# Performance work log

Measured on AMD Instinct MI355X. Metric: run time of the kernel, lower is better.

Reference implementation:

```python
import jax, jax.numpy as jnp
import numpy as np

N_NODES = 512
STATE_DIM = 16
MESSAGE_DIM = 32
HID_MSG = 64
HID_RO = 64
N_STEPS = 5


def setup_inputs() -> dict:
    key = jax.random.key(0)
    ks = jax.random.split(key, 16)
    s, m, hm, hr = STATE_DIM, MESSAGE_DIM, HID_MSG, HID_RO
    gru_in = s + m
    k_gru = 1.0 / np.sqrt(s)
    inp = {
        'J': jax.random.normal(ks[0], (N_NODES, N_NODES), jnp.float32),
        'b': jax.random.normal(ks[1], (N_NODES,), jnp.float32),
        # message MLP (torch init: weight ~ N(0, 0.1), bias = 0)
        'W1': 0.1 * jax.random.normal(ks[2], (hm, 2 * s + 3), jnp.float32),
        'b1': jnp.zeros((hm,), jnp.float32),
        'W2': 0.1 * jax.random.normal(ks[3], (hm, hm), jnp.float32),
        'b2': jnp.zeros((hm,), jnp.float32),
        'W3': 0.1 * jax.random.normal(ks[4], (m, hm), jnp.float32),
        'b3': jnp.zeros((m,), jnp.float32),
        # GRUCell params (torch default: U(-1/sqrt(hidden), 1/sqrt(hidden)))
        'W_ih': jax.random.uniform(ks[5], (3 * s, gru_in), jnp.float32, -k_gru, k_gru),
        'b_ih': jnp.zeros((3 * s,), jnp.float32),
        'W_hh': jax.random.uniform(ks[6], (3 * s, s), jnp.float32, -k_gru, k_gru),
        'b_hh': jnp.zeros((3 * s,), jnp.float32),
        # readout MLP
        'Wr1': 0.1 * jax.random.normal(ks[7], (hr, s), jnp.float32),
        'br1': jnp.zeros((hr,), jnp.float32),
        'Wr2': 0.1 * jax.random.normal(ks[8], (hr, hr), jnp.float32),
        'br2': jnp.zeros((hr,), jnp.float32),
        'Wr3': 0.1 * jax.random.normal(ks[9], (2, hr), jnp.float32),
        'br3': jnp.zeros((2,), jnp.float32),
    }
    return inp


def _gru_cell(x, h, W_ih, b_ih, W_hh, b_hh):
    s = h.shape[-1]
    gi = x @ W_ih.T + b_ih  # (n, 3s)
    gh = h @ W_hh.T + b_hh  # (n, 3s)
    ir, iz, in_ = gi[:, :s], gi[:, s:2 * s], gi[:, 2 * s:]
    hr, hz, hn = gh[:, :s], gh[:, s:2 * s], gh[:, 2 * s:]
    r = jax.nn.sigmoid(ir + hr)
    z = jax.nn.sigmoid(iz + hz)
    n = jnp.tanh(in_ + r * hn)
    return (1.0 - z) * n + z * h


def reference(J, b, W1, b1, W2, b2, W3, b3, W_ih, b_ih, W_hh, b_hh,
              Wr1, br1, Wr2, br2, Wr3, br3):
    n = J.shape[0]
    s = W_hh.shape[1]
    # Split first message-MLP layer by input blocks [h_i | h_j | J_ij | b_i | b_j]
    # so we never materialize the (n, n, 2s+3) feature tensor.
    W1_hi = W1[:, :s]            # (hm, s)
    W1_hj = W1[:, s:2 * s]       # (hm, s)
    w_J = W1[:, 2 * s]           # (hm,)
    w_bi = W1[:, 2 * s + 1]      # (hm,)
    w_bj = W1[:, 2 * s + 2]      # (hm,)
    # static per-pair part of layer-1 preactivation: (n, n, hm)
    static1 = (J[:, :, None] * w_J
               + b[:, None, None] * w_bi
               + b[None, :, None] * w_bj
               + b1)

    h0 = jnp.zeros((n, s), jnp.float32)

    def step(h, _):
        pre = (h @ W1_hi.T)[:, None, :] + (h @ W1_hj.T)[None, :, :] + static1
        x = jax.nn.relu(pre)                      # (n, n, hm)
        x = jax.nn.relu(x @ W2.T + b2)            # (n, n, hm)
        msg = x @ W3.T + b3                       # (n, n, m)
        m_j = msg.sum(axis=0)                     # sum over i -> (n, m)
        gru_in = jnp.concatenate([h, m_j], axis=1)
        h_new = _gru_cell(gru_in, h, W_ih, b_ih, W_hh, b_hh)
        return h_new, None

    h, _ = jax.lax.scan(step, h0, None, length=N_STEPS)

    y = jax.nn.relu(h @ Wr1.T + br1)
    y = jax.nn.relu(y @ Wr2.T + br2)
    y = jax.nn.sigmoid(y @ Wr3.T + br3)           # (n, 2)
    y = y / jnp.sum(y, axis=1, keepdims=True)
    return y
```

## Files before the change

### kernel.cpp

```cpp
#include <hip/hip_runtime.h>
#include <hip/hip_bf16.h>

#define NSTEPS 5
#define ABUFSZ 32768

typedef __attribute__((ext_vector_type(8))) short short8;
typedef __attribute__((ext_vector_type(4))) float floatx4;

static __device__ __forceinline__ unsigned pk2bf(float a, float b) {
    __hip_bfloat162 h = __float22bfloat162_rn(make_float2(a, b));
    return *reinterpret_cast<unsigned*>(&h);
}

static __device__ __forceinline__ void store_wt4(float* addr, floatx4 v) {
    __asm__ volatile("global_store_dwordx4 %0, %1, off sc0 sc1"
                     :: "v"(addr), "v"(v) : "memory");
}
static __device__ __forceinline__ void store_wt1(float* addr, float v) {
    __asm__ volatile("global_store_dword %0, %1, off sc0 sc1"
                     :: "v"(addr), "v"(v) : "memory");
}

struct Params {
    const float *J, *b, *W1, *b1, *W2, *b2, *W3, *b3;
    const float *W_ih, *b_ih, *W_hh, *b_hh;
    const float *Wr1, *br1, *Wr2, *br2, *Wr3, *br3;
    float *out;
    float *aBase;
    float *Jt;
    unsigned *bar;
};

static __device__ __forceinline__ void gbar(unsigned* bar, unsigned ph) {
    __builtin_amdgcn_s_waitcnt(0);
    __syncthreads();
    if (threadIdx.x == 0) {
        const int g = blockIdx.x & 7;
        unsigned old = __hip_atomic_fetch_add(&bar[g * 16], 1u, __ATOMIC_RELAXED,
                                              __HIP_MEMORY_SCOPE_AGENT);
        if (old == 64u * ph - 1u) {
            unsigned mo = __hip_atomic_fetch_add(&bar[128], 1u, __ATOMIC_RELAXED,
                                                 __HIP_MEMORY_SCOPE_AGENT);
            if (mo == 8u * ph - 1u)
                __hip_atomic_store(&bar[144], ph, __ATOMIC_RELAXED,
                                   __HIP_MEMORY_SCOPE_AGENT);
        }
        while (__hip_atomic_load(&bar[144], __ATOMIC_RELAXED,
                                 __HIP_MEMORY_SCOPE_AGENT) < ph)
            __builtin_amdgcn_s_sleep(2);
    }
    __syncthreads();
    __asm__ volatile("" ::: "memory");
}

__global__ __launch_bounds__(256, 2) void ggnn_fused(Params p)
{
    const int tid = threadIdx.x;
    const int l = tid & 63, w = tid >> 6;
    const int m = l & 15, q = l >> 4;
    const int j = blockIdx.x;

    __shared__ __align__(16) float smTile[64][65];
    __shared__ __align__(16) float smJ[512];
    __shared__ __align__(16) float smW1hi[64][16];
    __shared__ __align__(16) float smW1hj[64][16];
    __shared__ __align__(16) float smwJ[64], smwbi[64], smwbj[64], smb1[64];
    __shared__ __align__(16) float smC[64];
    __shared__ __align__(16) float smA[64];
    __shared__ __align__(16) float smH[16];
    __shared__ __align__(16) float smWave[4][64];
    __shared__ __align__(16) float smMacc[64];
    __shared__ __align__(16) float smGin[48];
    __shared__ __align__(16) float smGi[48], smGh[48];
    __shared__ __align__(16) float smY[64], smY2[64];
    __shared__ float smR[2];

    if (blockIdx.x < 64) {
        int ti = blockIdx.x >> 3, tj = blockIdx.x & 7;
        for (int pp = 0; pp < 16; ++pp) {
            int e = pp * 256 + tid; int r = e >> 6, c = e & 63;
            smTile[r][c] = p.J[(ti * 64 + r) * 512 + tj * 64 + c];
        }
        __syncthreads();
        for (int pp = 0; pp < 16; ++pp) {
            int e = pp * 256 + tid; int r = e >> 6, c = e & 63;
            store_wt1(p.Jt + (tj * 64 + r) * 512 + ti * 64 + c, smTile[c][r]);
        }
    }

    if (tid < 64) {
        int o = tid;
        #pragma unroll
        for (int s = 0; s < 16; ++s) {
            smW1hi[o][s] = p.W1[o * 35 + s];
            smW1hj[o][s] = p.W1[o * 35 + 16 + s];
        }
        smwJ[o]  = p.W1[o * 35 + 32];
        smwbi[o] = p.W1[o * 35 + 33];
        smwbj[o] = p.W1[o * 35 + 34];
        smb1[o]  = p.b1[o];
    }

    short8 bfw[4][2];
    float b2n[4];
    {
        const floatx4* W2v = (const floatx4*)p.W2;
        #pragma unroll
        for (int nt = 0; nt < 4; ++nt) {
            int n = nt * 16 + m;
            #pragma unroll
            for (int ks = 0; ks < 2; ++ks) {
                int kb = ks * 32 + q * 8;
                floatx4 f0 = W2v[n * 16 + (kb >> 2)];
                floatx4 f1 = W2v[n * 16 + (kb >> 2) + 1];
                union { short8 s; unsigned u[4]; } t;
                t.u[0] = pk2bf(f0[0], f0[1]); t.u[1] = pk2bf(f0[2], f0[3]);
                t.u[2] = pk2bf(f1[0], f1[1]); t.u[3] = pk2bf(f1[2], f1[3]);
                bfw[nt][ks] = t.s;
            }
            b2n[nt] = p.b2[nt * 16 + m];
        }
    }
    __syncthreads();

    const float bj = p.b[j];

    floatx4 wva, wvb, wvc, wvd;
    {
        const floatx4* wv4 = (const floatx4*)smwJ;
        wva = wv4[q * 2];     wvb = wv4[q * 2 + 1];
        wvc = wv4[8 + q * 2]; wvd = wv4[8 + q * 2 + 1];
    }

    if (tid < 64) smC[tid] = bj * smwbj[tid] + smb1[tid];
    if (tid < 16) {
        floatx4 v;
        #pragma unroll
        for (int e = 0; e < 4; ++e) v[e] = bj * smwbi[tid * 4 + e];
        store_wt4(p.aBase + j * 64 + tid * 4, v);
        smH[tid] = 0.f;
    }

    gbar(p.bar, 1);

    if (tid < 128) ((floatx4*)smJ)[tid] = ((const floatx4*)p.Jt)[j * 128 + tid];
    __syncthreads();

    for (int t = 0; t < NSTEPS; ++t) {
        const float* aIn = p.aBase + t * ABUFSZ;
        const floatx4* c4 = (const floatx4*)smC;
        floatx4 cva = c4[q*2], cvb = c4[q*2+1], cvc = c4[8+q*2], cvd = c4[8+q*2+1];

        floatx4 acc[4];
        #pragma unroll
        for (int nt = 0; nt < 4; ++nt) acc[nt] = (floatx4){0.f,0.f,0.f,0.f};

        const floatx4* a4 = (const floatx4*)aIn;

        for (int c8 = 0; c8 < 8; ++c8) {
            int i = w * 128 + c8 * 16 + m;
            float Jij = smJ[i];
            floatx4 av0 = a4[i*16 + q*2],     av1 = a4[i*16 + q*2 + 1];
            floatx4 av2 = a4[i*16 + 8 + q*2], av3 = a4[i*16 + 8 + q*2 + 1];
            floatx4 x0, x1, x2, x3;
            #pragma unroll
            for (int e = 0; e < 4; ++e) {
                x0[e] = fmaxf(fmaf(Jij, wva[e], av0[e]) + cva[e], 0.f);
                x1[e] = fmaxf(fmaf(Jij, wvb[e], av1[e]) + cvb[e], 0.f);
                x2[e] = fmaxf(fmaf(Jij, wvc[e], av2[e]) + cvc[e], 0.f);
                x3[e] = fmaxf(fmaf(Jij, wvd[e], av3[e]) + cvd[e], 0.f);
            }
            union { short8 s; unsigned u[4]; } fa0, fa1;
            fa0.u[0] = pk2bf(x0[0], x0[1]); fa0.u[1] = pk2bf(x0[2], x0[3]);
            fa0.u[2] = pk2bf(x1[0], x1[1]); fa0.u[3] = pk2bf(x1[2], x1[3]);
            fa1.u[0] = pk2bf(x2[0], x2[1]); fa1.u[1] = pk2bf(x2[2], x2[3]);
            fa1.u[2] = pk2bf(x3[0], x3[1]); fa1.u[3] = pk2bf(x3[2], x3[3]);
            #pragma unroll
            for (int nt = 0; nt < 4; ++nt) {
                floatx4 d = {0.f,0.f,0.f,0.f};
                d = __builtin_amdgcn_mfma_f32_16x16x32_bf16(fa0.s, bfw[nt][0], d, 0, 0, 0);
                d = __builtin_amdgcn_mfma_f32_16x16x32_bf16(fa1.s, bfw[nt][1], d, 0, 0, 0);
                #pragma unroll
                for (int r = 0; r < 4; ++r)
                    acc[nt][r] += fmaxf(d[r] + b2n[nt], 0.f);
            }
        }

        #pragma unroll
        for (int nt = 0; nt < 4; ++nt) {
            float v = acc[nt][0] + acc[nt][1] + acc[nt][2] + acc[nt][3];
            v += __shfl_xor(v, 16);
            v += __shfl_xor(v, 32);
            if (l < 16) smWave[w][nt*16 + l] = v;
        }
        if (tid < 16) smGin[tid] = smH[tid];
        __syncthreads();
        if (tid < 64) smMacc[tid] = smWave[0][tid] + smWave[1][tid]
                                  + smWave[2][tid] + smWave[3][tid];
        __syncthreads();

        {
            int o = tid >> 3, pp = tid & 7;
            const floatx4* W3v = (const floatx4*)p.W3;
            floatx4 wv0 = W3v[o*16 + pp*2], wv1 = W3v[o*16 + pp*2 + 1];
            float part = 0.f;
            #pragma unroll
            for (int e = 0; e < 4; ++e) {
                part = fmaf(wv0[e], smMacc[pp*8 + e], part);
                part = fmaf(wv1[e], smMacc[pp*8 + 4 + e], part);
            }
            part += __shfl_xor(part, 1);
            part += __shfl_xor(part, 2);
            part += __shfl_xor(part, 4);
            if (pp == 0) smGin[16 + o] = part + 512.f * p.b3[o];
        }
        __syncthreads();

        if (tid < 192) {
            int o = tid >> 2, pp = tid & 3;
            const floatx4* Wv = (const floatx4*)p.W_ih;
            floatx4 w0 = Wv[o*12 + pp*3], w1 = Wv[o*12 + pp*3 + 1], w2 = Wv[o*12 + pp*3 + 2];
            int k0 = pp * 12;
            float part = 0.f;
            #pragma unroll
            for (int e = 0; e < 4; ++e) {
                part = fmaf(w0[e], smGin[k0 + e], part);
                part = fmaf(w1[e], smGin[k0 + 4 + e], part);
                part = fmaf(w2[e], smGin[k0 + 8 + e], part);
            }
            part += __shfl_xor(part, 1);
            part += __shfl_xor(part, 2);
            if (pp == 0) smGi[o] = part + p.b_ih[o];
        } else if (tid < 240) {
            int o = tid - 192;
            const floatx4* Wv = (const floatx4*)p.W_hh;
            floatx4 w0 = Wv[o*4], w1 = Wv[o*4+1], w2 = Wv[o*4+2], w3 = Wv[o*4+3];
            float s = p.b_hh[o];
            #pragma unroll
            for (int e = 0; e < 4; ++e) {
                s = fmaf(w0[e], smGin[e],      s);
                s = fmaf(w1[e], smGin[4 + e],  s);
                s = fmaf(w2[e], smGin[8 + e],  s);
                s = fmaf(w3[e], smGin[12 + e], s);
            }
            smGh[o] = s;
        }
        __syncthreads();

        if (tid < 16) {
            float r = 1.f / (1.f + __expf(-(smGi[tid] + smGh[tid])));
            float z = 1.f / (1.f + __expf(-(smGi[16+tid] + smGh[16+tid])));
            float n = tanhf(smGi[32+tid] + r * smGh[32+tid]);
            smH[tid] = (1.f - z) * n + z * smGin[tid];
        }
        __syncthreads();

        if (t < NSTEPS - 1) {
            if (tid < 128) {
                int o = tid & 63, sel = tid >> 6;
                const floatx4* Wv = (const floatx4*)(sel ? &smW1hj[0][0] : &smW1hi[0][0]);
                const floatx4* h4 = (const floatx4*)smH;
                floatx4 w0 = Wv[o*4], w1 = Wv[o*4+1], w2 = Wv[o*4+2], w3 = Wv[o*4+3];
                float s = 0.f;
                #pragma unroll
                for (int e = 0; e < 4; ++e) {
                    s = fmaf(w0[e], h4[0][e], s);
                    s = fmaf(w1[e], h4[1][e], s);
                    s = fmaf(w2[e], h4[2][e], s);
                    s = fmaf(w3[e], h4[3][e], s);
                }
                if (sel == 0) smA[o] = s + bj * smwbi[o];
                else          smC[o] = s + bj * smwbj[o] + smb1[o];
            }
            __syncthreads();
            if (tid < 16) {
                float* aNext = p.aBase + (t + 1) * ABUFSZ;
                store_wt4(aNext + j * 64 + tid * 4, ((floatx4*)smA)[tid]);
            }
            gbar(p.bar, (unsigned)(t + 2));
        }
    }

    if (tid < 64) {
        const floatx4* Wv = (const floatx4*)p.Wr1;
        const floatx4* h4 = (const floatx4*)smH;
        floatx4 w0 = Wv[tid*4], w1 = Wv[tid*4+1], w2 = Wv[tid*4+2], w3 = Wv[tid*4+3];
        float s = p.br1[tid];
        #pragma unroll
        for (int e = 0; e < 4; ++e) {
            s = fmaf(w0[e], h4[0][e], s);
            s = fmaf(w1[e], h4[1][e], s);
            s = fmaf(w2[e], h4[2][e], s);
            s = fmaf(w3[e], h4[3][e], s);
        }
        smY[tid] = fmaxf(s, 0.f);
    }
    __syncthreads();
    {
        int o = tid >> 2, pp = tid & 3;
        const floatx4* Wv = (const floatx4*)p.Wr2;
        const floatx4* y4 = (const floatx4*)smY;
        floatx4 w0 = Wv[o*16 + pp*4],     w1 = Wv[o*16 + pp*4 + 1];
        floatx4 w2 = Wv[o*16 + pp*4 + 2], w3 = Wv[o*16 + pp*4 + 3];
        float part = 0.f;
        #pragma unroll
        for (int e = 0; e < 4; ++e) {
            part = fmaf(w0[e], y4[pp*4][e] * 0.f + smY[pp*16 + e],      part);
            part = fmaf(w1[e], smY[pp*16 + 4 + e],  part);
            part = fmaf(w2[e], smY[pp*16 + 8 + e],  part);
            part = fmaf(w3[e], smY[pp*16 + 12 + e], part);
        }
        part += __shfl_xor(part, 1);
        part += __shfl_xor(part, 2);
        if (pp == 0) smY2[o] = fmaxf(part + p.br2[o], 0.f);
    }
    __syncthreads();
    if (tid < 128) {
        int ot = tid >> 6, pp = tid & 63;
        float part = p.Wr3[ot*64 + pp] * smY2[pp];
        part += __shfl_xor(part, 1);
        part += __shfl_xor(part, 2);
        part += __shfl_xor(part, 4);
        part += __shfl_xor(part, 8);
        part += __shfl_xor(part, 16);
        part += __shfl_xor(part, 32);
        if (pp == 0) smR[ot] = part + p.br3[ot];
    }
    __syncthreads();
    if (tid == 0) {
        float e0 = 1.f / (1.f + __expf(-smR[0]));
        float e1 = 1.f / (1.f + __expf(-smR[1]));
        float tsum = e0 + e1;
        p.out[j*2]     = e0 / tsum;
        p.out[j*2 + 1] = e1 / tsum;
    }
}

extern "C" void kernel_launch(void* const* d_in, const int* in_sizes, int n_in,
                              void* d_out, int out_size, void* d_ws, size_t ws_size,
                              hipStream_t stream)
{
    Params par;
    par.J    = (const float*)d_in[0];
    par.b    = (const float*)d_in[1];
    par.W1   = (const float*)d_in[2];
    par.b1   = (const float*)d_in[3];
    par.W2   = (const float*)d_in[4];
    par.b2   = (const float*)d_in[5];
    par.W3   = (const float*)d_in[6];
    par.b3   = (const float*)d_in[7];
    par.W_ih = (const float*)d_in[8];
    par.b_ih = (const float*)d_in[9];
    par.W_hh = (const float*)d_in[10];
    par.b_hh = (const float*)d_in[11];
    par.Wr1  = (const float*)d_in[12];
    par.br1  = (const float*)d_in[13];
    par.Wr2  = (const float*)d_in[14];
    par.br2  = (const float*)d_in[15];
    par.Wr3  = (const float*)d_in[16];
    par.br3  = (const float*)d_in[17];
    par.out  = (float*)d_out;

    float* ws = (float*)d_ws;
    par.aBase = ws;
    par.Jt    = ws + NSTEPS * ABUFSZ;
    par.bar   = (unsigned*)(ws + NSTEPS * ABUFSZ + 262144);

    hipMemsetAsync(par.bar, 0, 1024, stream);
    hipLaunchKernelGGL(ggnn_fused, dim3(512), dim3(256), 0, stream, par);
}
```

Before: 163.8 us.

## Drop J transpose pre-pass and initial grid barrier; use 512-thread blocks

Removes the cooperative J transpose through global memory along with the first grid-wide barrier. Each block now reads its column of J directly with strided loads and keeps b in shared memory. Step 0 computes the h=0 layer-1 preactivation locally from b_i instead of reading a global buffer. Blocks grow to 512 threads (8 waves), so each wave processes half as many rows, and the wave reduction and W3 matvec are adjusted to match. This cuts one grid barrier and a global round trip, at the cost of uncoalesced column loads and higher register pressure under the new launch bounds.

```diff
diff --git a/kernel.cpp b/kernel.cpp
--- a/kernel.cpp
+++ b/kernel.cpp
@@ -14,10 +14,6 @@
 
 static __device__ __forceinline__ void store_wt4(float* addr, floatx4 v) {
     __asm__ volatile("global_store_dwordx4 %0, %1, off sc0 sc1"
-                     :: "v"(addr), "v"(v) : "memory");
-}
-static __device__ __forceinline__ void store_wt1(float* addr, float v) {
-    __asm__ volatile("global_store_dword %0, %1, off sc0 sc1"
                      :: "v"(addr), "v"(v) : "memory");
 }
 
@@ -27,7 +23,6 @@
     const float *Wr1, *br1, *Wr2, *br2, *Wr3, *br3;
     float *out;
     float *aBase;
-    float *Jt;
     unsigned *bar;
 };
 
@@ -53,41 +48,30 @@
     __asm__ volatile("" ::: "memory");
 }
 
-__global__ __launch_bounds__(256, 2) void ggnn_fused(Params p)
+__global__ __launch_bounds__(512, 4) void ggnn_fused(Params p)
 {
     const int tid = threadIdx.x;
     const int l = tid & 63, w = tid >> 6;
     const int m = l & 15, q = l >> 4;
     const int j = blockIdx.x;
 
-    __shared__ __align__(16) float smTile[64][65];
     __shared__ __align__(16) float smJ[512];
+    __shared__ __align__(16) float smB[512];
     __shared__ __align__(16) float smW1hi[64][16];
     __shared__ __align__(16) float smW1hj[64][16];
     __shared__ __align__(16) float smwJ[64], smwbi[64], smwbj[64], smb1[64];
     __shared__ __align__(16) float smC[64];
     __shared__ __align__(16) float smA[64];
     __shared__ __align__(16) float smH[16];
-    __shared__ __align__(16) float smWave[4][64];
+    __shared__ __align__(16) float smWave[8][64];
     __shared__ __align__(16) float smMacc[64];
     __shared__ __align__(16) float smGin[48];
     __shared__ __align__(16) float smGi[48], smGh[48];
     __shared__ __align__(16) float smY[64], smY2[64];
     __shared__ float smR[2];
 
-    if (blockIdx.x < 64) {
-        int ti = blockIdx.x >> 3, tj = blockIdx.x & 7;
-        for (int pp = 0; pp < 16; ++pp) {
-            int e = pp * 256 + tid; int r = e >> 6, c = e & 63;
-            smTile[r][c] = p.J[(ti * 64 + r) * 512 + tj * 64 + c];
-        }
-        __syncthreads();
-        for (int pp = 0; pp < 16; ++pp) {
-            int e = pp * 256 + tid; int r = e >> 6, c = e & 63;
-            store_wt1(p.Jt + (tj * 64 + r) * 512 + ti * 64 + c, smTile[c][r]);
-        }
-    }
-
+    smJ[tid] = p.J[tid * 512 + j];
+    smB[tid] = p.b[tid];
     if (tid < 64) {
         int o = tid;
         #pragma unroll
@@ -123,7 +107,9 @@
     }
     __syncthreads();
 
-    const float bj = p.b[j];
+    const float bj = smB[j];
+    if (tid < 64) smC[tid] = bj * smwbj[tid] + smb1[tid];
+    if (tid < 16) smH[tid] = 0.f;
 
     floatx4 wva, wvb, wvc, wvd;
     {
@@ -131,23 +117,9 @@
         wva = wv4[q * 2];     wvb = wv4[q * 2 + 1];
         wvc = wv4[8 + q * 2]; wvd = wv4[8 + q * 2 + 1];
     }
-
-    if (tid < 64) smC[tid] = bj * smwbj[tid] + smb1[tid];
-    if (tid < 16) {
-        floatx4 v;
-        #pragma unroll
-        for (int e = 0; e < 4; ++e) v[e] = bj * smwbi[tid * 4 + e];
-        store_wt4(p.aBase + j * 64 + tid * 4, v);
-        smH[tid] = 0.f;
-    }
-
-    gbar(p.bar, 1);
-
-    if (tid < 128) ((floatx4*)smJ)[tid] = ((const floatx4*)p.Jt)[j * 128 + tid];
     __syncthreads();
 
     for (int t = 0; t < NSTEPS; ++t) {
-        const float* aIn = p.aBase + t * ABUFSZ;
         const floatx4* c4 = (const floatx4*)smC;
         floatx4 cva = c4[q*2], cvb = c4[q*2+1], cvc = c4[8+q*2], cvd = c4[8+q*2+1];
 
@@ -155,34 +127,65 @@
         #pragma unroll
         for (int nt = 0; nt < 4; ++nt) acc[nt] = (floatx4){0.f,0.f,0.f,0.f};
 
-        const floatx4* a4 = (const floatx4*)aIn;
-
-        for (int c8 = 0; c8 < 8; ++c8) {
-            int i = w * 128 + c8 * 16 + m;
-            float Jij = smJ[i];
-            floatx4 av0 = a4[i*16 + q*2],     av1 = a4[i*16 + q*2 + 1];
-            floatx4 av2 = a4[i*16 + 8 + q*2], av3 = a4[i*16 + 8 + q*2 + 1];
-            floatx4 x0, x1, x2, x3;
-            #pragma unroll
-            for (int e = 0; e < 4; ++e) {
-                x0[e] = fmaxf(fmaf(Jij, wva[e], av0[e]) + cva[e], 0.f);
-                x1[e] = fmaxf(fmaf(Jij, wvb[e], av1[e]) + cvb[e], 0.f);
-                x2[e] = fmaxf(fmaf(Jij, wvc[e], av2[e]) + cvc[e], 0.f);
-                x3[e] = fmaxf(fmaf(Jij, wvd[e], av3[e]) + cvd[e], 0.f);
-            }
-            union { short8 s; unsigned u[4]; } fa0, fa1;
-            fa0.u[0] = pk2bf(x0[0], x0[1]); fa0.u[1] = pk2bf(x0[2], x0[3]);
-            fa0.u[2] = pk2bf(x1[0], x1[1]); fa0.u[3] = pk2bf(x1[2], x1[3]);
-            fa1.u[0] = pk2bf(x2[0], x2[1]); fa1.u[1] = pk2bf(x2[2], x2[3]);
-            fa1.u[2] = pk2bf(x3[0], x3[1]); fa1.u[3] = pk2bf(x3[2], x3[3]);
-            #pragma unroll
-            for (int nt = 0; nt < 4; ++nt) {
-                floatx4 d = {0.f,0.f,0.f,0.f};
-                d = __builtin_amdgcn_mfma_f32_16x16x32_bf16(fa0.s, bfw[nt][0], d, 0, 0, 0);
-                d = __builtin_amdgcn_mfma_f32_16x16x32_bf16(fa1.s, bfw[nt][1], d, 0, 0, 0);
-                #pragma unroll
-                for (int r = 0; r < 4; ++r)
-                    acc[nt][r] += fmaxf(d[r] + b2n[nt], 0.f);
+        if (t == 0) {
+            const floatx4* wb4 = (const floatx4*)smwbi;
+            floatx4 bva = wb4[q*2], bvb = wb4[q*2+1], bvc = wb4[8+q*2], bvd = wb4[8+q*2+1];
+            for (int c8 = 0; c8 < 4; ++c8) {
+                int i = w * 64 + c8 * 16 + m;
+                float Jij = smJ[i];
+                float bi  = smB[i];
+                floatx4 x0, x1, x2, x3;
+                #pragma unroll
+                for (int e = 0; e < 4; ++e) {
+                    x0[e] = fmaxf(fmaf(Jij, wva[e], fmaf(bi, bva[e], cva[e])), 0.f);
+                    x1[e] = fmaxf(fmaf(Jij, wvb[e], fmaf(bi, bvb[e], cvb[e])), 0.f);
+                    x2[e] = fmaxf(fmaf(Jij, wvc[e], fmaf(bi, bvc[e], cvc[e])), 0.f);
+                    x3[e] = fmaxf(fmaf(Jij, wvd[e], fmaf(bi, bvd[e], cvd[e])), 0.f);
+                }
+                union { short8 s; unsigned u[4]; } fa0, fa1;
+                fa0.u[0] = pk2bf(x0[0], x0[1]); fa0.u[1] = pk2bf(x0[2], x0[3]);
+                fa0.u[2] = pk2bf(x1[0], x1[1]); fa0.u[3] = pk2bf(x1[2], x1[3]);
+                fa1.u[0] = pk2bf(x2[0], x2[1]); fa1.u[1] = pk2bf(x2[2], x2[3]);
+                fa1.u[2] = pk2bf(x3[0], x3[1]); fa1.u[3] = pk2bf(x3[2], x3[3]);
+                #pragma unroll
+                for (int nt = 0; nt < 4; ++nt) {
+                    floatx4 d = {0.f,0.f,0.f,0.f};
+                    d = __builtin_amdgcn_mfma_f32_16x16x32_bf16(fa0.s, bfw[nt][0], d, 0, 0, 0);
+                    d = __builtin_amdgcn_mfma_f32_16x16x32_bf16(fa1.s, bfw[nt][1], d, 0, 0, 0);
+                    #pragma unroll
+                    for (int r = 0; r < 4; ++r)
+                        acc[nt][r] += fmaxf(d[r] + b2n[nt], 0.f);
+                }
+            }
+        } else {
+            const floatx4* a4 = (const floatx4*)(p.aBase + t * ABUFSZ);
+            for (int c8 = 0; c8 < 4; ++c8) {
+                int i = w * 64 + c8 * 16 + m;
+                float Jij = smJ[i];
+                floatx4 av0 = a4[i*16 + q*2],     av1 = a4[i*16 + q*2 + 1];
+                floatx4 av2 = a4[i*16 + 8 + q*2], av3 = a4[i*16 + 8 + q*2 + 1];
+                floatx4 x0, x1, x2, x3;
+                #pragma unroll
+                for (int e = 0; e < 4; ++e) {
+                    x0[e] = fmaxf(fmaf(Jij, wva[e], av0[e]) + cva[e], 0.f);
+                    x1[e] = fmaxf(fmaf(Jij, wvb[e], av1[e]) + cvb[e], 0.f);
+                    x2[e] = fmaxf(fmaf(Jij, wvc[e], av2[e]) + cvc[e], 0.f);
+                    x3[e] = fmaxf(fmaf(Jij, wvd[e], av3[e]) + cvd[e], 0.f);
+                }
+                union { short8 s; unsigned u[4]; } fa0, fa1;
+                fa0.u[0] = pk2bf(x0[0], x0[1]); fa0.u[1] = pk2bf(x0[2], x0[3]);
+                fa0.u[2] = pk2bf(x1[0], x1[1]); fa0.u[3] = pk2bf(x1[2], x1[3]);
+                fa1.u[0] = pk2bf(x2[0], x2[1]); fa1.u[1] = pk2bf(x2[2], x2[3]);
+                fa1.u[2] = pk2bf(x3[0], x3[1]); fa1.u[3] = pk2bf(x3[2], x3[3]);
+                #pragma unroll
+                for (int nt = 0; nt < 4; ++nt) {
+                    floatx4 d = {0.f,0.f,0.f,0.f};
+                    d = __builtin_amdgcn_mfma_f32_16x16x32_bf16(fa0.s, bfw[nt][0], d, 0, 0, 0);
+                    d = __builtin_amdgcn_mfma_f32_16x16x32_bf16(fa1.s, bfw[nt][1], d, 0, 0, 0);
+                    #pragma unroll
+                    for (int r = 0; r < 4; ++r)
+                        acc[nt][r] += fmaxf(d[r] + b2n[nt], 0.f);
+                }
             }
         }
 
@@ -195,23 +198,25 @@
         }
         if (tid < 16) smGin[tid] = smH[tid];
         __syncthreads();
-        if (tid < 64) smMacc[tid] = smWave[0][tid] + smWave[1][tid]
-                                  + smWave[2][tid] + smWave[3][tid];
+        if (tid < 64) {
+            float s = smWave[0][tid];
+            #pragma unroll
+            for (int ww = 1; ww < 8; ++ww) s += smWave[ww][tid];
+            smMacc[tid] = s;
+        }
         __syncthreads();
 
         {
-            int o = tid >> 3, pp = tid & 7;
+            int o = tid >> 4, pp = tid & 15;
             const floatx4* W3v = (const floatx4*)p.W3;
-            floatx4 wv0 = W3v[o*16 + pp*2], wv1 = W3v[o*16 + pp*2 + 1];
-            float part = 0.f;
-            #pragma unroll
-            for (int e = 0; e < 4; ++e) {
-                part = fmaf(wv0[e], smMacc[pp*8 + e], part);
-                part = fmaf(wv1[e], smMacc[pp*8 + 4 + e], part);
-            }
+            floatx4 wv0 = W3v[o*16 + pp];
+            const floatx4* mac4 = (const floatx4*)smMacc;
+            floatx4 mv = mac4[pp];
+            float part = wv0[0]*mv[0] + wv0[1]*mv[1] + wv0[2]*mv[2] + wv0[3]*mv[3];
             part += __shfl_xor(part, 1);
             part += __shfl_xor(part, 2);
             part += __shfl_xor(part, 4);
+            part += __shfl_xor(part, 8);
             if (pp == 0) smGin[16 + o] = part + 512.f * p.b3[o];
         }
         __syncthreads();
@@ -277,7 +282,7 @@
                 float* aNext = p.aBase + (t + 1) * ABUFSZ;
                 store_wt4(aNext + j * 64 + tid * 4, ((floatx4*)smA)[tid]);
             }
-            gbar(p.bar, (unsigned)(t + 2));
+            gbar(p.bar, (unsigned)(t + 1));
         }
     }
 
@@ -296,16 +301,15 @@
         smY[tid] = fmaxf(s, 0.f);
     }
     __syncthreads();
-    {
+    if (tid < 256) {
         int o = tid >> 2, pp = tid & 3;
         const floatx4* Wv = (const floatx4*)p.Wr2;
-        const floatx4* y4 = (const floatx4*)smY;
         floatx4 w0 = Wv[o*16 + pp*4],     w1 = Wv[o*16 + pp*4 + 1];
         floatx4 w2 = Wv[o*16 + pp*4 + 2], w3 = Wv[o*16 + pp*4 + 3];
         float part = 0.f;
         #pragma unroll
         for (int e = 0; e < 4; ++e) {
-            part = fmaf(w0[e], y4[pp*4][e] * 0.f + smY[pp*16 + e],      part);
+            part = fmaf(w0[e], smY[pp*16 + e],      part);
             part = fmaf(w1[e], smY[pp*16 + 4 + e],  part);
             part = fmaf(w2[e], smY[pp*16 + 8 + e],  part);
             part = fmaf(w3[e], smY[pp*16 + 12 + e], part);
@@ -363,9 +367,8 @@
 
     float* ws = (float*)d_ws;
     par.aBase = ws;
-    par.Jt    = ws + NSTEPS * ABUFSZ;
-    par.bar   = (unsigned*)(ws + NSTEPS * ABUFSZ + 262144);
+    par.bar   = (unsigned*)(ws + NSTEPS * ABUFSZ);
 
     hipMemsetAsync(par.bar, 0, 1024, stream);
-    hipLaunchKernelGGL(ggnn_fused, dim3(512), dim3(256), 0, stream, par);
-}
+    hipLaunchKernelGGL(ggnn_fused, dim3(512), dim3(512), 0, stream, par);
+}
```

New measurement: 240.5 us. +46.8%, slower.
